# Kernel tuning notes

Hardware: AMD Instinct MI355X
Metric: run time of the kernel (lower is better)

## Reference

```python
import jax, jax.numpy as jnp
import numpy as np

SFREQ = 100
NPERSEG = 100  # min(n_times=200, 100)
NOVERLAP = NPERSEG // 2

# periodic hann window (scipy get_window('hann', N) with sym=False)
_WIN_NP = 0.5 - 0.5 * np.cos(2.0 * np.pi * np.arange(NPERSEG) / NPERSEG)
_WIN_SQ_SUM = float(np.sum(_WIN_NP ** 2))
_FREQS = np.fft.rfftfreq(NPERSEG, 1.0 / SFREQ)  # 0..50 Hz, 51 bins
_BANDS = [(0.5, 4.0), (4.0, 8.0), (8.0, 13.0), (13.0, 30.0)]  # delta/theta/alpha/beta
_BAND_IDX = [np.where((_FREQS >= lo) & (_FREQS <= hi))[0] for lo, hi in _BANDS]


def welch_band_features(x):
    """Batched Welch PSD band powers. x: (B,C,T) -> (B, C*4)."""
    B, C, T = x.shape
    step = NPERSEG - NOVERLAP
    n_seg = (T - NPERSEG) // step + 1
    seg_idx = np.arange(n_seg)[:, None] * step + np.arange(NPERSEG)  # (S, L)
    segs = x[..., seg_idx]                              # (B,C,S,L)
    segs = segs - segs.mean(-1, keepdims=True)          # detrend='constant'
    win = jnp.asarray(_WIN_NP, x.dtype)
    spec = jnp.fft.rfft(segs * win, axis=-1)            # (B,C,S,F)
    scale = 1.0 / (SFREQ * _WIN_SQ_SUM)
    psd = (spec.real ** 2 + spec.imag ** 2) * scale
    psd = psd.at[..., 1:-1].multiply(2.0)               # one-sided, nfft even
    psd = psd.mean(-2)                                  # average over segments -> (B,C,F)
    feats = jnp.stack([psd[..., idx].mean(-1) for idx in _BAND_IDX], axis=-1)  # (B,C,4)
    return feats.reshape(B, C * 4)


def setup_inputs() -> dict:
    key = jax.random.key(0)
    ks = jax.random.split(key, 16)
    B, C, T = 2048, 129, 200
    red = C // 8  # 16
    s = 0.05
    inp = {
        "x": jax.random.normal(ks[0], (B, C, T), jnp.float32),
        # channel attention fc (no bias)
        "w_att1": jax.random.normal(ks[1], (C, red), jnp.float32) * s,
        "w_att2": jax.random.normal(ks[2], (red, C), jnp.float32) * s,
        # stand-in EEGNeX backbone: time-mean pool + linear C->64
        "w_bb": jax.random.normal(ks[3], (C, 64), jnp.float32) * s,
        "b_bb": jnp.zeros((64,), jnp.float32),
        # freq encoder
        "w_fe1": jax.random.normal(ks[4], (C * 4, 128), jnp.float32) * s,
        "b_fe1": jnp.zeros((128,), jnp.float32),
        "w_fe2": jax.random.normal(ks[5], (128, 64), jnp.float32) * s,
        "b_fe2": jnp.zeros((64,), jnp.float32),
        # head
        "w_h1": jax.random.normal(ks[6], (128, 128), jnp.float32) * s,
        "b_h1": jnp.zeros((128,), jnp.float32),
        "w_h2": jax.random.normal(ks[7], (128, 64), jnp.float32) * s,
        "b_h2": jnp.zeros((64,), jnp.float32),
        "w_h3": jax.random.normal(ks[8], (64, 1), jnp.float32) * s,
        "b_h3": jnp.zeros((1,), jnp.float32),
    }
    return inp


def reference(x, w_att1, w_att2, w_bb, b_bb, w_fe1, b_fe1, w_fe2, b_fe2,
              w_h1, b_h1, w_h2, b_h2, w_h3, b_h3):
    # --- channel attention ---
    avg = x.mean(-1)                                    # (B,C)
    mx = x.max(-1)                                      # (B,C)
    fc = lambda v: jax.nn.relu(v @ w_att1) @ w_att2
    att = jax.nn.sigmoid(fc(avg) + fc(mx))[..., None]   # (B,C,1)
    x_att = x * att
    # --- backbone (stand-in for EEGNeXBase): time pool + linear ---
    time_feat = jax.nn.relu(x_att.mean(-1) @ w_bb + b_bb)  # (B,64)
    # --- frequency branch (computed from raw x, detached in original) ---
    freq = welch_band_features(jax.lax.stop_gradient(x))   # (B, C*4)
    freq = jax.nn.relu(freq @ w_fe1 + b_fe1)
    freq = jax.nn.relu(freq @ w_fe2 + b_fe2)               # (B,64)
    # --- head ---
    h = jnp.concatenate([time_feat, freq], axis=1)         # (B,128)
    h = jax.nn.relu(h @ w_h1 + b_h1)
    h = jax.nn.relu(h @ w_h2 + b_h2)
    return h @ w_h3 + b_h3                                  # (B,1)
```

## Files before the change

### kernel.cpp

```cpp
#include <hip/hip_runtime.h>
#include <math.h>

constexpr int BB = 2048;
constexpr int CC = 129;
constexpr int TT = 200;
constexpr int NPAIR = BB * CC;
constexpr int PPB = 64;
constexpr int XSTR = 204;

constexpr int OFF_AVG = 8192;
constexpr int OFF_MX  = OFF_AVG + NPAIR;
constexpr int OFF_FT  = OFF_MX + NPAIR;

__global__ void kInit(float2* __restrict__ tab) {
    int i = blockIdx.x * 256 + threadIdx.x;
    if (i >= 3000) return;
    int r = i / 100, t = i % 100;
    int ph = ((r + 1) * t) % 100;
    const float C = 0.06283185307179587f;
    float w = 0.5f - 0.5f * cosf(C * (float)t);
    float ang = C * (float)ph;
    tab[i] = make_float2(w * cosf(ang), w * sinf(ang));
}

template<int KB, int NB>
__device__ __forceinline__ void dft_wave(const float* __restrict__ xp,
                                         const float* __restrict__ tabg,
                                         float* __restrict__ bs,
                                         float mu0, float mu1, float mu2) {
    const float* trow = tabg + (KB - 1) * 200;
    float re[NB][3], im[NB][3];
    #pragma unroll
    for (int b = 0; b < NB; b++)
        #pragma unroll
        for (int s = 0; s < 3; s++) { re[b][s] = 0.f; im[b][s] = 0.f; }

    #pragma unroll 5
    for (int t0 = 0; t0 < 100; t0 += 4) {
        float4 a  = *(const float4*)(xp + t0);
        float2 b0 = *(const float2*)(xp + t0 + 50);
        float2 b1 = *(const float2*)(xp + t0 + 52);
        float4 c  = *(const float4*)(xp + t0 + 100);
        float xa[4] = {a.x, a.y, a.z, a.w};
        float xb[4] = {b0.x, b0.y, b1.x, b1.y};
        float xc[4] = {c.x, c.y, c.z, c.w};
        #pragma unroll
        for (int b = 0; b < NB; b++) {
            float4 w0 = *(const float4*)(trow + b * 200 + 2 * t0);
            float4 w1 = *(const float4*)(trow + b * 200 + 2 * t0 + 4);
            float cs[4] = {w0.x, w0.z, w1.x, w1.z};
            float sn[4] = {w0.y, w0.w, w1.y, w1.w};
            #pragma unroll
            for (int u = 0; u < 4; u++) {
                re[b][0] += xa[u] * cs[u];  im[b][0] += xa[u] * sn[u];
                re[b][1] += xb[u] * cs[u];  im[b][1] += xb[u] * sn[u];
                re[b][2] += xc[u] * cs[u];  im[b][2] += xc[u] * sn[u];
            }
        }
    }

    if (KB == 1) {
        re[0][0] += 25.f * mu0;
        re[0][1] += 25.f * mu1;
        re[0][2] += 25.f * mu2;
    }

    float s0 = 0.f, s1 = 0.f, s2 = 0.f, s3 = 0.f;
    #pragma unroll
    for (int b = 0; b < NB; b++) {
        int k = KB + b;
        float v = re[b][0] * re[b][0] + im[b][0] * im[b][0]
                + re[b][1] * re[b][1] + im[b][1] * im[b][1]
                + re[b][2] * re[b][2] + im[b][2] * im[b][2];
        if (k >= 1  && k <= 4)  s0 += v;
        if (k >= 4  && k <= 8)  s1 += v;
        if (k >= 8  && k <= 13) s2 += v;
        if (k >= 13)            s3 += v;
    }
    if (KB <= 4)                       atomicAdd(&bs[0], s0);
    if (KB <= 8 && KB + NB - 1 >= 4)   atomicAdd(&bs[1], s1);
    if (KB <= 13 && KB + NB - 1 >= 8)  atomicAdd(&bs[2], s2);
    if (KB + NB - 1 >= 13)             atomicAdd(&bs[3], s3);
}

__global__ __launch_bounds__(256, 3) void kA(const float* __restrict__ x,
                                             const float* __restrict__ tabg,
                                             float* __restrict__ avg,
                                             float* __restrict__ mxg,
                                             float* __restrict__ feat) {
    __shared__ __align__(16) float xs[PPB * XSTR];
    __shared__ float bsum[PPB][4];

    const int tid = threadIdx.x;
    const int blk = blockIdx.x;

    {
        const float4* xg = (const float4*)(x + (size_t)blk * PPB * TT);
        for (int i = tid; i < 3200; i += 256) {
            float4 v = xg[i];
            int p = i / 50, t4 = (i % 50) * 4;
            *(float4*)(xs + p * XSTR + t4) = v;
        }
    }
    ((float*)bsum)[tid] = 0.f;
    __syncthreads();

    const int wv = tid >> 6, p = tid & 63;
    const float* xp = xs + p * XSTR;
    float* bs = bsum[p];

    float mu0 = 0.f, mu1 = 0.f, mu2 = 0.f;
    if (wv == 0) {
        float h0 = 0.f, h1 = 0.f, h2 = 0.f, h3 = 0.f, m = -3.4e38f;
        #pragma unroll
        for (int i = 0; i < 12; i++) {
            float4 v = *(const float4*)(xp + i * 4);
            h0 += (v.x + v.y) + (v.z + v.w);
            m = fmaxf(m, fmaxf(fmaxf(v.x, v.y), fmaxf(v.z, v.w)));
        }
        {   float4 v = *(const float4*)(xp + 48);
            h0 += v.x + v.y; h1 += v.z + v.w;
            m = fmaxf(m, fmaxf(fmaxf(v.x, v.y), fmaxf(v.z, v.w))); }
        #pragma unroll
        for (int i = 13; i < 25; i++) {
            float4 v = *(const float4*)(xp + i * 4);
            h1 += (v.x + v.y) + (v.z + v.w);
            m = fmaxf(m, fmaxf(fmaxf(v.x, v.y), fmaxf(v.z, v.w)));
        }
        #pragma unroll
        for (int i = 25; i < 37; i++) {
            float4 v = *(const float4*)(xp + i * 4);
            h2 += (v.x + v.y) + (v.z + v.w);
            m = fmaxf(m, fmaxf(fmaxf(v.x, v.y), fmaxf(v.z, v.w)));
        }
        {   float4 v = *(const float4*)(xp + 148);
            h2 += v.x + v.y; h3 += v.z + v.w;
            m = fmaxf(m, fmaxf(fmaxf(v.x, v.y), fmaxf(v.z, v.w))); }
        #pragma unroll
        for (int i = 38; i < 50; i++) {
            float4 v = *(const float4*)(xp + i * 4);
            h3 += (v.x + v.y) + (v.z + v.w);
            m = fmaxf(m, fmaxf(fmaxf(v.x, v.y), fmaxf(v.z, v.w)));
        }
        int pair = blk * PPB + p;
        avg[pair] = (h0 + h1 + h2 + h3) * (1.f / 200.f);
        mxg[pair] = m;
        mu0 = (h0 + h1) * 0.01f; mu1 = (h1 + h2) * 0.01f; mu2 = (h2 + h3) * 0.01f;
    }

    switch (wv) {
        case 0: dft_wave<1,  6>(xp, tabg, bs, mu0, mu1, mu2); break;
        case 1: dft_wave<7,  8>(xp, tabg, bs, 0, 0, 0); break;
        case 2: dft_wave<15, 8>(xp, tabg, bs, 0, 0, 0); break;
        default: dft_wave<23, 8>(xp, tabg, bs, 0, 0, 0); break;
    }

    __syncthreads();
    {
        int pp = tid >> 2, bb = tid & 3;
        const float cnt[4] = {4.f, 5.f, 6.f, 18.f};
        feat[(size_t)(blk * PPB + pp) * 4 + bb] = bsum[pp][bb] * (2.f / (11250.f * cnt[bb]));
    }
}

__global__ __launch_bounds__(256, 8) void kB(const float* __restrict__ avg,
                                             const float* __restrict__ mxv,
                                             const float* __restrict__ feat,
                                             const float* __restrict__ w_att1,
                                             const float* __restrict__ w_att2,
                                             const float* __restrict__ w_bb,
                                             const float* __restrict__ b_bb,
                                             const float* __restrict__ w_fe1,
                                             const float* __restrict__ b_fe1,
                                             const float* __restrict__ w_fe2,
                                             const float* __restrict__ b_fe2,
                                             const float* __restrict__ w_h1,
                                             const float* __restrict__ b_h1,
                                             const float* __restrict__ w_h2,
                                             const float* __restrict__ b_h2,
                                             const float* __restrict__ w_h3,
                                             const float* __restrict__ b_h3,
                                             float* __restrict__ out) {
    __shared__ float s_avg[132], s_mx[132], s_fq[520];
    __shared__ float s_t1a[16], s_t1b[16], s_t1[16];
    __shared__ float s_v[132];
    __shared__ float s_tf[2][64];
    __shared__ float s_p1[2][128];
    __shared__ float s_f1[128];
    __shared__ float s_p2[4][64];
    __shared__ float s_h[128];
    __shared__ float s_pg1[2][128];
    __shared__ float s_g1[128];
    __shared__ float s_pg2[4][64];

    const int b = blockIdx.x;
    const int tid = threadIdx.x;

    for (int i = tid; i < 129; i += 256) { s_avg[i] = avg[b * 129 + i]; s_mx[i] = mxv[b * 129 + i]; }
    for (int i = tid; i < 516; i += 256) s_fq[i] = feat[(size_t)b * 516 + i];
    __syncthreads();

    if (tid < 32) {
        int h = tid & 15;
        const float* src = (tid >= 16) ? s_mx : s_avg;
        float acc = 0.f;
        #pragma unroll 4
        for (int c = 0; c < 129; c++) acc += src[c] * w_att1[c * 16 + h];
        ((tid >= 16) ? s_t1b : s_t1a)[h] = fmaxf(acc, 0.f);
    }
    __syncthreads();
    if (tid < 16) s_t1[tid] = s_t1a[tid] + s_t1b[tid];
    __syncthreads();

    if (tid < 129) {
        float l = 0.f;
        #pragma unroll
        for (int j = 0; j < 16; j++) l += s_t1[j] * w_att2[j * 129 + tid];
        s_v[tid] = s_avg[tid] / (1.f + expf(-l));
    }
    __syncthreads();

    if (tid < 128) {
        int o = tid & 63, ks = tid >> 6;
        int i0 = ks ? 65 : 0, i1 = ks ? 129 : 65;
        float acc = 0.f;
        #pragma unroll 4
        for (int i = i0; i < i1; i++) acc += s_v[i] * w_bb[i * 64 + o];
        s_tf[ks][o] = acc;
    }
    {
        int o = tid & 127, ks = tid >> 7;
        float acc = 0.f;
        #pragma unroll 4
        for (int i = ks * 258; i < ks * 258 + 258; i++) acc += s_fq[i] * w_fe1[i * 128 + o];
        s_p1[ks][o] = acc;
    }
    __syncthreads();
    if (tid < 64) s_h[tid] = fmaxf(s_tf[0][tid] + s_tf[1][tid] + b_bb[tid], 0.f);
    if (tid >= 128) { int o = tid - 128; s_f1[o] = fmaxf(s_p1[0][o] + s_p1[1][o] + b_fe1[o], 0.f); }
    __syncthreads();

    {
        int o = tid & 63, ks = tid >> 6;
        float acc = 0.f;
        #pragma unroll 4
        for (int i = ks * 32; i < ks * 32 + 32; i++) acc += s_f1[i] * w_fe2[i * 64 + o];
        s_p2[ks][o] = acc;
    }
    __syncthreads();
    if (tid < 64) s_h[64 + tid] = fmaxf(s_p2[0][tid] + s_p2[1][tid] + s_p2[2][tid] + s_p2[3][tid] + b_fe2[tid], 0.f);
    __syncthreads();

    {
        int o = tid & 127, ks = tid >> 7;
        float acc = 0.f;
        #pragma unroll 4
        for (int i = ks * 64; i < ks * 64 + 64; i++) acc += s_h[i] * w_h1[i * 128 + o];
        s_pg1[ks][o] = acc;
    }
    __syncthreads();
    if (tid < 128) s_g1[tid] = fmaxf(s_pg1[0][tid] + s_pg1[1][tid] + b_h1[tid], 0.f);
    __syncthreads();

    {
        int o = tid & 63, ks = tid >> 6;
        float acc = 0.f;
        #pragma unroll 4
        for (int i = ks * 32; i < ks * 32 + 32; i++) acc += s_g1[i] * w_h2[i * 64 + o];
        s_pg2[ks][o] = acc;
    }
    __syncthreads();

    if (tid < 64) {
        float g2 = fmaxf(s_pg2[0][tid] + s_pg2[1][tid] + s_pg2[2][tid] + s_pg2[3][tid] + b_h2[tid], 0.f);
        float pz = g2 * w_h3[tid];
        for (int off = 32; off >= 1; off >>= 1) pz += __shfl_xor(pz, off, 64);
        if (tid == 0) out[b] = pz + b_h3[0];
    }
}

extern "C" void kernel_launch(void* const* d_in, const int* in_sizes, int n_in,
                              void* d_out, int out_size, void* d_ws, size_t ws_size,
                              hipStream_t stream) {
    const float* x      = (const float*)d_in[0];
    const float* w_att1 = (const float*)d_in[1];
    const float* w_att2 = (const float*)d_in[2];
    const float* w_bb   = (const float*)d_in[3];
    const float* b_bb   = (const float*)d_in[4];
    const float* w_fe1  = (const float*)d_in[5];
    const float* b_fe1  = (const float*)d_in[6];
    const float* w_fe2  = (const float*)d_in[7];
    const float* b_fe2  = (const float*)d_in[8];
    const float* w_h1   = (const float*)d_in[9];
    const float* b_h1   = (const float*)d_in[10];
    const float* w_h2   = (const float*)d_in[11];
    const float* b_h2   = (const float*)d_in[12];
    const float* w_h3   = (const float*)d_in[13];
    const float* b_h3   = (const float*)d_in[14];

    float* ws = (float*)d_ws;
    float2* tab = (float2*)ws;
    float* avg = ws + OFF_AVG;
    float* mxv = ws + OFF_MX;
    float* feat = ws + OFF_FT;

    kInit<<<12, 256, 0, stream>>>(tab);
    kA<<<NPAIR / PPB, 256, 0, stream>>>(x, (const float*)tab, avg, mxv, feat);
    kB<<<BB, 256, 0, stream>>>(avg, mxv, feat,
                               w_att1, w_att2, w_bb, b_bb,
                               w_fe1, b_fe1, w_fe2, b_fe2,
                               w_h1, b_h1, w_h2, b_h2, w_h3, b_h3,
                               (float*)d_out);
}
```

Measured before the change: 508.4 us.

## Compute Welch DFT with split-bf16 MFMA matrix multiply instead of scalar FMAs

```diff
diff --git a/kernel.cpp b/kernel.cpp
--- a/kernel.cpp
+++ b/kernel.cpp
@@ -12,154 +12,178 @@
 constexpr int OFF_MX  = OFF_AVG + NPAIR;
 constexpr int OFF_FT  = OFF_MX + NPAIR;
 
-__global__ void kInit(float2* __restrict__ tab) {
-    int i = blockIdx.x * 256 + threadIdx.x;
-    if (i >= 3000) return;
-    int r = i / 100, t = i % 100;
-    int ph = ((r + 1) * t) % 100;
-    const float C = 0.06283185307179587f;
-    float w = 0.5f - 0.5f * cosf(C * (float)t);
-    float ang = C * (float)ph;
-    tab[i] = make_float2(w * cosf(ang), w * sinf(ang));
+typedef __bf16 bf16x8 __attribute__((ext_vector_type(8)));
+typedef float  f32x4  __attribute__((ext_vector_type(4)));
+
+union BFU { int4 v; bf16x8 b; };
+union BSU { __bf16 b; unsigned short u; };
+
+__global__ void kInit(unsigned short* __restrict__ bfr) {
+    int tid = blockIdx.x * 256 + threadIdx.x;
+    if (tid >= 16384) return;
+    int i    = tid & 7;
+    int lane = (tid >> 3) & 63;
+    int h    = (tid >> 9) & 1;
+    int nt   = (tid >> 10) & 3;
+    int ks   = tid >> 12;
+    int k = ks * 32 + (lane >> 4) * 8 + i;
+    int n = nt * 16 + (lane & 15);
+    float v = 0.f;
+    if (k < 100) {
+        if (n < 60) {
+            int kb = (n >> 1) + 1;
+            const float C = 0.06283185307179587f;
+            float w = 0.5f - 0.5f * cosf(C * (float)k);
+            int ph = (kb * k) % 100;
+            float ang = C * (float)ph;
+            v = w * ((n & 1) ? sinf(ang) : cosf(ang));
+        } else if (n == 60) {
+            v = 0.01f;
+        }
+    }
+    __bf16 hb = (__bf16)v;
+    BSU out;
+    if (h == 0) out.b = hb;
+    else        out.b = (__bf16)(v - (float)hb);
+    bfr[tid] = out.u;
 }
 
-template<int KB, int NB>
-__device__ __forceinline__ void dft_wave(const float* __restrict__ xp,
-                                         const float* __restrict__ tabg,
-                                         float* __restrict__ bs,
-                                         float mu0, float mu1, float mu2) {
-    const float* trow = tabg + (KB - 1) * 200;
-    float re[NB][3], im[NB][3];
-    #pragma unroll
-    for (int b = 0; b < NB; b++)
-        #pragma unroll
-        for (int s = 0; s < 3; s++) { re[b][s] = 0.f; im[b][s] = 0.f; }
-
-    #pragma unroll 5
-    for (int t0 = 0; t0 < 100; t0 += 4) {
-        float4 a  = *(const float4*)(xp + t0);
-        float2 b0 = *(const float2*)(xp + t0 + 50);
-        float2 b1 = *(const float2*)(xp + t0 + 52);
-        float4 c  = *(const float4*)(xp + t0 + 100);
-        float xa[4] = {a.x, a.y, a.z, a.w};
-        float xb[4] = {b0.x, b0.y, b1.x, b1.y};
-        float xc[4] = {c.x, c.y, c.z, c.w};
-        #pragma unroll
-        for (int b = 0; b < NB; b++) {
-            float4 w0 = *(const float4*)(trow + b * 200 + 2 * t0);
-            float4 w1 = *(const float4*)(trow + b * 200 + 2 * t0 + 4);
-            float cs[4] = {w0.x, w0.z, w1.x, w1.z};
-            float sn[4] = {w0.y, w0.w, w1.y, w1.w};
-            #pragma unroll
-            for (int u = 0; u < 4; u++) {
-                re[b][0] += xa[u] * cs[u];  im[b][0] += xa[u] * sn[u];
-                re[b][1] += xb[u] * cs[u];  im[b][1] += xb[u] * sn[u];
-                re[b][2] += xc[u] * cs[u];  im[b][2] += xc[u] * sn[u];
-            }
-        }
-    }
-
-    if (KB == 1) {
-        re[0][0] += 25.f * mu0;
-        re[0][1] += 25.f * mu1;
-        re[0][2] += 25.f * mu2;
-    }
-
-    float s0 = 0.f, s1 = 0.f, s2 = 0.f, s3 = 0.f;
-    #pragma unroll
-    for (int b = 0; b < NB; b++) {
-        int k = KB + b;
-        float v = re[b][0] * re[b][0] + im[b][0] * im[b][0]
-                + re[b][1] * re[b][1] + im[b][1] * im[b][1]
-                + re[b][2] * re[b][2] + im[b][2] * im[b][2];
-        if (k >= 1  && k <= 4)  s0 += v;
-        if (k >= 4  && k <= 8)  s1 += v;
-        if (k >= 8  && k <= 13) s2 += v;
-        if (k >= 13)            s3 += v;
-    }
-    if (KB <= 4)                       atomicAdd(&bs[0], s0);
-    if (KB <= 8 && KB + NB - 1 >= 4)   atomicAdd(&bs[1], s1);
-    if (KB <= 13 && KB + NB - 1 >= 8)  atomicAdd(&bs[2], s2);
-    if (KB + NB - 1 >= 13)             atomicAdd(&bs[3], s3);
-}
-
-__global__ __launch_bounds__(256, 3) void kA(const float* __restrict__ x,
-                                             const float* __restrict__ tabg,
+__global__ __launch_bounds__(256, 2) void kA(const float* __restrict__ x,
+                                             const unsigned short* __restrict__ bfr,
                                              float* __restrict__ avg,
                                              float* __restrict__ mxg,
                                              float* __restrict__ feat) {
-    __shared__ __align__(16) float xs[PPB * XSTR];
-    __shared__ float bsum[PPB][4];
+    __shared__ __align__(16) float xs[PPB * XSTR + 32];
 
     const int tid = threadIdx.x;
     const int blk = blockIdx.x;
 
     {
         const float4* xg = (const float4*)(x + (size_t)blk * PPB * TT);
-        for (int i = tid; i < 3200; i += 256) {
-            float4 v = xg[i];
-            int p = i / 50, t4 = (i % 50) * 4;
-            *(float4*)(xs + p * XSTR + t4) = v;
-        }
-    }
-    ((float*)bsum)[tid] = 0.f;
-    __syncthreads();
-
-    const int wv = tid >> 6, p = tid & 63;
-    const float* xp = xs + p * XSTR;
-    float* bs = bsum[p];
-
-    float mu0 = 0.f, mu1 = 0.f, mu2 = 0.f;
-    if (wv == 0) {
-        float h0 = 0.f, h1 = 0.f, h2 = 0.f, h3 = 0.f, m = -3.4e38f;
-        #pragma unroll
-        for (int i = 0; i < 12; i++) {
-            float4 v = *(const float4*)(xp + i * 4);
-            h0 += (v.x + v.y) + (v.z + v.w);
-            m = fmaxf(m, fmaxf(fmaxf(v.x, v.y), fmaxf(v.z, v.w)));
-        }
-        {   float4 v = *(const float4*)(xp + 48);
-            h0 += v.x + v.y; h1 += v.z + v.w;
-            m = fmaxf(m, fmaxf(fmaxf(v.x, v.y), fmaxf(v.z, v.w))); }
-        #pragma unroll
-        for (int i = 13; i < 25; i++) {
-            float4 v = *(const float4*)(xp + i * 4);
-            h1 += (v.x + v.y) + (v.z + v.w);
-            m = fmaxf(m, fmaxf(fmaxf(v.x, v.y), fmaxf(v.z, v.w)));
-        }
-        #pragma unroll
-        for (int i = 25; i < 37; i++) {
-            float4 v = *(const float4*)(xp + i * 4);
-            h2 += (v.x + v.y) + (v.z + v.w);
-            m = fmaxf(m, fmaxf(fmaxf(v.x, v.y), fmaxf(v.z, v.w)));
-        }
-        {   float4 v = *(const float4*)(xp + 148);
-            h2 += v.x + v.y; h3 += v.z + v.w;
-            m = fmaxf(m, fmaxf(fmaxf(v.x, v.y), fmaxf(v.z, v.w))); }
-        #pragma unroll
-        for (int i = 38; i < 50; i++) {
-            float4 v = *(const float4*)(xp + i * 4);
-            h3 += (v.x + v.y) + (v.z + v.w);
-            m = fmaxf(m, fmaxf(fmaxf(v.x, v.y), fmaxf(v.z, v.w)));
-        }
-        int pair = blk * PPB + p;
-        avg[pair] = (h0 + h1 + h2 + h3) * (1.f / 200.f);
-        mxg[pair] = m;
-        mu0 = (h0 + h1) * 0.01f; mu1 = (h1 + h2) * 0.01f; mu2 = (h2 + h3) * 0.01f;
-    }
-
-    switch (wv) {
-        case 0: dft_wave<1,  6>(xp, tabg, bs, mu0, mu1, mu2); break;
-        case 1: dft_wave<7,  8>(xp, tabg, bs, 0, 0, 0); break;
-        case 2: dft_wave<15, 8>(xp, tabg, bs, 0, 0, 0); break;
-        default: dft_wave<23, 8>(xp, tabg, bs, 0, 0, 0); break;
-    }
-
-    __syncthreads();
-    {
-        int pp = tid >> 2, bb = tid & 3;
+        #pragma unroll
+        for (int it = 0; it < 13; it++) {
+            int idx = tid + it * 256;
+            if (idx < 3200) {
+                float4 v = xg[idx];
+                int p = idx / 50, t4 = (idx % 50) * 4;
+                *(float4*)(xs + p * XSTR + t4) = v;
+            }
+        }
+        if (tid < 64) *(float4*)(xs + tid * XSTR + 200) = float4{0.f, 0.f, 0.f, 0.f};
+        if (tid < 32) xs[PPB * XSTR + tid] = 0.f;
+    }
+
+    bf16x8 Bh[4][4], Bl[4][4];
+    {
+        const int4* bg = (const int4*)bfr;
+        int ln = tid & 63;
+        #pragma unroll
+        for (int ks = 0; ks < 4; ks++)
+            #pragma unroll
+            for (int nt = 0; nt < 4; nt++) {
+                BFU uh, ul;
+                uh.v = bg[((ks * 4 + nt) * 2 + 0) * 64 + ln];
+                ul.v = bg[((ks * 4 + nt) * 2 + 1) * 64 + ln];
+                Bh[ks][nt] = uh.b;
+                Bl[ks][nt] = ul.b;
+            }
+    }
+    __syncthreads();
+
+    {
+        int p = tid >> 2, q = tid & 3;
+        const float* src = xs + p * XSTR + q * 50;
+        float m = -3.4e38f;
+        #pragma unroll
+        for (int i = 0; i < 25; i++) {
+            float2 v = *(const float2*)(src + i * 2);
+            m = fmaxf(m, fmaxf(v.x, v.y));
+        }
+        m = fmaxf(m, __shfl_xor(m, 1, 64));
+        m = fmaxf(m, __shfl_xor(m, 2, 64));
+        if (q == 0) mxg[blk * PPB + p] = m;
+    }
+
+    const int wv = tid >> 6, lane = tid & 63;
+    const int quad = lane >> 4, mrow = lane & 15;
+    f32x4 acc[3][4];
+    #pragma unroll
+    for (int a = 0; a < 3; a++)
+        #pragma unroll
+        for (int b = 0; b < 4; b++) acc[a][b] = f32x4{0.f, 0.f, 0.f, 0.f};
+
+    #pragma unroll
+    for (int mi = 0; mi < 3; mi++) {
+        int mt = wv * 3 + mi;
+        int r = mt * 16 + mrow;
+        int pair = r / 3;
+        int seg = r - pair * 3;
+        const float* abase = xs + pair * XSTR + seg * 50 + quad * 8;
+        #pragma unroll
+        for (int ks = 0; ks < 4; ks++) {
+            const float* s = abase + ks * 32;
+            float2 f0 = *(const float2*)(s);
+            float2 f1 = *(const float2*)(s + 2);
+            float2 f2 = *(const float2*)(s + 4);
+            float2 f3 = *(const float2*)(s + 6);
+            float f[8] = {f0.x, f0.y, f1.x, f1.y, f2.x, f2.y, f3.x, f3.y};
+            bf16x8 Ah, Al;
+            #pragma unroll
+            for (int i = 0; i < 8; i++) {
+                __bf16 hb = (__bf16)f[i];
+                Ah[i] = hb;
+                Al[i] = (__bf16)(f[i] - (float)hb);
+            }
+            #pragma unroll
+            for (int nt = 0; nt < 4; nt++) {
+                acc[mi][nt] = __builtin_amdgcn_mfma_f32_16x16x32_bf16(Al, Bh[ks][nt], acc[mi][nt], 0, 0, 0);
+                acc[mi][nt] = __builtin_amdgcn_mfma_f32_16x16x32_bf16(Ah, Bl[ks][nt], acc[mi][nt], 0, 0, 0);
+                acc[mi][nt] = __builtin_amdgcn_mfma_f32_16x16x32_bf16(Ah, Bh[ks][nt], acc[mi][nt], 0, 0, 0);
+            }
+        }
+    }
+    __syncthreads();
+
+    float* sp = xs;
+    #pragma unroll
+    for (int mi = 0; mi < 3; mi++) {
+        int mt = wv * 3 + mi;
+        #pragma unroll
+        for (int nt = 0; nt < 4; nt++) {
+            int col = nt * 16 + mrow;
+            #pragma unroll
+            for (int i = 0; i < 4; i++) {
+                int row = mt * 16 + quad * 4 + i;
+                sp[row * 66 + col] = acc[mi][nt][i];
+            }
+        }
+    }
+    __syncthreads();
+
+    {
+        int p = tid >> 2, bnd = tid & 3;
+        const int c0[4] = {0, 6, 14, 24};
+        const int c1[4] = {7, 15, 25, 59};
+        float sum = 0.f;
+        #pragma unroll
+        for (int s = 0; s < 3; s++) {
+            const float* row = sp + (p * 3 + s) * 66;
+            float mu = row[60];
+            int lo = c0[bnd];
+            if (bnd == 0) {
+                float v = row[0] + 25.f * mu;
+                sum += v * v;
+                lo = 1;
+            }
+            for (int c = lo; c <= c1[bnd]; c++) {
+                float v = row[c];
+                sum += v * v;
+            }
+        }
+        if (bnd == 0)
+            avg[blk * PPB + p] = (sp[(p * 3) * 66 + 60] + sp[(p * 3 + 2) * 66 + 60]) * 0.5f;
         const float cnt[4] = {4.f, 5.f, 6.f, 18.f};
-        feat[(size_t)(blk * PPB + pp) * 4 + bb] = bsum[pp][bb] * (2.f / (11250.f * cnt[bb]));
+        feat[(size_t)(blk * PPB + p) * 4 + bnd] = sum * (2.f / (11250.f * cnt[bnd]));
     }
 }
 
@@ -299,13 +323,13 @@
     const float* b_h3   = (const float*)d_in[14];
 
     float* ws = (float*)d_ws;
-    float2* tab = (float2*)ws;
+    unsigned short* bfr = (unsigned short*)ws;
     float* avg = ws + OFF_AVG;
     float* mxv = ws + OFF_MX;
     float* feat = ws + OFF_FT;
 
-    kInit<<<12, 256, 0, stream>>>(tab);
-    kA<<<NPAIR / PPB, 256, 0, stream>>>(x, (const float*)tab, avg, mxv, feat);
+    kInit<<<64, 256, 0, stream>>>(bfr);
+    kA<<<NPAIR / PPB, 256, 0, stream>>>(x, bfr, avg, mxv, feat);
     kB<<<BB, 256, 0, stream>>>(avg, mxv, feat,
                                w_att1, w_att2, w_bb, b_bb,
                                w_fe1, b_fe1, w_fe2, b_fe2,
```

Result: faster. 474.1 us (-6.7%).
